# Performance work log

Measured on AMD Instinct MI355X. Metric: run time of the kernel, lower is better.

## Reference

```python
import jax, jax.numpy as jnp
import numpy as np

UNITS = 256


def setup_inputs() -> dict:
    key = jax.random.key(0)
    ks = jax.random.split(key, 9)
    B, H, W, C = 8, 64, 64, UNITS
    x = jax.random.normal(ks[0], (B, H, W, C), dtype=jnp.float32)
    # 1x1 Conv2D == per-pixel linear: weight [C_in, C_out], bias [C_out]
    def lin(k):
        return jax.random.normal(k, (C, UNITS), dtype=jnp.float32) * (2.0 / C) ** 0.5
    return {
        "x": x,
        "wq": lin(ks[1]), "bq": jnp.zeros((UNITS,), jnp.float32),
        "wk": lin(ks[2]), "bk": jnp.zeros((UNITS,), jnp.float32),
        "wv": lin(ks[3]), "bv": jnp.zeros((UNITS,), jnp.float32),
        "wp": lin(ks[4]), "bp": jnp.zeros((UNITS,), jnp.float32),
    }


def reference(x, wq, bq, wk, bk, wv, bv, wp, bp):
    B, H, W, C = x.shape
    N = H * W
    scale = jnp.asarray(UNITS, jnp.float32) ** -0.5
    xf = x.reshape(B, N, C)  # 1x1 conv == matmul over channels
    q = xf @ wq + bq
    k = xf @ wk + bk
    v = xf @ wv + bv
    # (b,h,w,c)x(b,H,W,c)->(b,h,w,H,W) flattened to (b,N,N)
    scores = jnp.einsum('bnc,bmc->bnm', q, k) * scale
    attn = jax.nn.softmax(scores, axis=-1)
    out = jnp.einsum('bnm,bmc->bnc', attn, v)
    proj = out @ wp + bp
    return x + proj.reshape(B, H, W, UNITS)
```

## Files before the change

kernel.cpp:

```cpp
#include <hip/hip_runtime.h>


typedef _Float16 half8 __attribute__((ext_vector_type(8)));
typedef _Float16 half4 __attribute__((ext_vector_type(4)));
typedef float f32x4 __attribute__((ext_vector_type(4)));
typedef float f32x16 __attribute__((ext_vector_type(16)));
typedef unsigned int u32x4 __attribute__((ext_vector_type(4)));
typedef unsigned int u32x2 __attribute__((ext_vector_type(2)));

#define MFMA16(a, b, c) __builtin_amdgcn_mfma_f32_16x16x32_f16((a), (b), (c), 0, 0, 0)
#define MFMA32(a, b, c) __builtin_amdgcn_mfma_f32_32x32x16_f16((a), (b), (c), 0, 0, 0)

#if __has_builtin(__builtin_amdgcn_exp2f)
#define EXP2(x) __builtin_amdgcn_exp2f(x)
#else
#define EXP2(x) exp2f(x)
#endif

#define QSCALE 0.09016843898f
#define ESHIFT 11.5415603f

__device__ __forceinline__ void lds_load16(const void* g, void* l) {
    __builtin_amdgcn_global_load_lds(
        (const __attribute__((address_space(1))) unsigned int*)g,
        (__attribute__((address_space(3))) unsigned int*)l, 16, 0, 0);
}

__global__ __launch_bounds__(256)
void wt_prep(const float* __restrict__ w0, const float* __restrict__ w1,
             const float* __restrict__ w2, const float* __restrict__ w3,
             _Float16* __restrict__ outw)
{
    __shared__ _Float16 sT[64 * 72];
    const int z = blockIdx.z;
    const float* W = (z == 0) ? w0 : (z == 1) ? w1 : (z == 2) ? w2 : w3;
    _Float16* O = outw + z * 65536;
    const int kb = blockIdx.x * 64, nb = blockIdx.y * 64;
    const int t = threadIdx.x;
    const int r = t >> 4, c4 = (t & 15) * 4;
#pragma unroll
    for (int i = 0; i < 4; ++i) {
        f32x4 ld = *(const f32x4*)(W + (size_t)(kb + r + i * 16) * 256 + nb + c4);
#pragma unroll
        for (int j = 0; j < 4; ++j) sT[(c4 + j) * 72 + r + i * 16] = (_Float16)ld[j];
    }
    __syncthreads();
#pragma unroll
    for (int i = 0; i < 4; ++i) {
        int n = r + i * 16;
        *(u32x2*)&O[(size_t)(nb + n) * 256 + kb + c4] = *(const u32x2*)&sT[n * 72 + c4];
    }
}

__global__ __launch_bounds__(256)
void qkv_gemm(const float* __restrict__ x, const _Float16* __restrict__ wt,
              const float* __restrict__ bq, const float* __restrict__ bk,
              const float* __restrict__ bv,
              _Float16* __restrict__ qo, _Float16* __restrict__ ko,
              _Float16* __restrict__ vo)
{
    __shared__ _Float16 smem[4 * 2560];
    _Float16* sA = smem;

    const int tid  = threadIdx.x;
    const int w    = tid >> 6;
    const int lane = tid & 63;
    const int quad = lane >> 4;
    const int l16  = lane & 15;
    const int m0   = blockIdx.x * 64;
    const int n0   = blockIdx.y * 64;
    const int rS = tid >> 2, cS = (tid & 3) << 3;

    const float* ap = x + (size_t)(m0 + rS) * 256 + cS;
    f32x4 a0 = *(const f32x4*)ap, a1 = *(const f32x4*)(ap + 4);
    u32x4 bst[3];
#pragma unroll
    for (int o = 0; o < 3; ++o)
        bst[o] = *(const u32x4*)(wt + o * 65536 + (size_t)(n0 + rS) * 256 + cS);

    f32x4 zero4 = {0.f, 0.f, 0.f, 0.f};
    f32x4 acc[3][4];
#pragma unroll
    for (int o = 0; o < 3; ++o)
#pragma unroll
        for (int mt = 0; mt < 4; ++mt) acc[o][mt] = zero4;

    for (int it = 0; it < 8; ++it) {
        __syncthreads();
        half8 t;
#pragma unroll
        for (int j = 0; j < 4; ++j) { t[j] = (_Float16)a0[j]; t[j + 4] = (_Float16)a1[j]; }
        *(half8*)&sA[rS * 40 + cS] = t;
#pragma unroll
        for (int o = 0; o < 3; ++o)
            *(u32x4*)&smem[2560 * (o + 1) + rS * 40 + cS] = bst[o];
        __syncthreads();
        if (it < 7) {
            int k0 = (it + 1) * 32;
            const float* ap2 = x + (size_t)(m0 + rS) * 256 + k0 + cS;
            a0 = *(const f32x4*)ap2; a1 = *(const f32x4*)(ap2 + 4);
#pragma unroll
            for (int o = 0; o < 3; ++o)
                bst[o] = *(const u32x4*)(wt + o * 65536 + (size_t)(n0 + rS) * 256 + k0 + cS);
        }
        half8 af[4];
#pragma unroll
        for (int mt = 0; mt < 4; ++mt)
            af[mt] = *(const half8*)&sA[(mt * 16 + l16) * 40 + quad * 8];
#pragma unroll
        for (int o = 0; o < 3; ++o) {
            half8 bf = *(const half8*)&smem[2560 * (o + 1) + (16 * w + l16) * 40 + quad * 8];
#pragma unroll
            for (int mt = 0; mt < 4; ++mt)
                acc[o][mt] = MFMA16(af[mt], bf, acc[o][mt]);
        }
    }

    const int col = n0 + 16 * w + l16;
#pragma unroll
    for (int mt = 0; mt < 4; ++mt) {
#pragma unroll
        for (int reg = 0; reg < 4; ++reg) {
            int row = m0 + 16 * mt + quad * 4 + reg;
            qo[(size_t)row * 256 + col] = (_Float16)((acc[0][mt][reg] + bq[col]) * QSCALE);
            ko[(size_t)row * 256 + col] = (_Float16)(acc[1][mt][reg] + bk[col]);
        }
    }
    __syncthreads();
    _Float16* sT = smem;
#pragma unroll
    for (int mt = 0; mt < 4; ++mt)
#pragma unroll
        for (int reg = 0; reg < 4; ++reg)
            sT[(16 * w + l16) * 72 + 16 * mt + quad * 4 + reg] =
                (_Float16)(acc[2][mt][reg] + bv[col]);
    __syncthreads();
    int ch = tid >> 2, po = (tid & 3) << 4;
    int bb = m0 >> 12, pix = m0 & 4095;
    _Float16* dst = vo + (size_t)bb * 1048576 + (size_t)(n0 + ch) * 4096 + pix + po;
    *(u32x4*)dst       = *(const u32x4*)&sT[ch * 72 + po];
    *(u32x4*)(dst + 8) = *(const u32x4*)&sT[ch * 72 + po + 8];
}

__global__ __launch_bounds__(256)
void proj_gemm(const _Float16* __restrict__ opart, const float* __restrict__ lpart,
               const _Float16* __restrict__ Wt, const float* __restrict__ bias,
               const float* __restrict__ resid, float* __restrict__ out)
{
    __shared__ _Float16 smem[2 * 2560];
    _Float16* sA = smem;
    _Float16* sB = smem + 2560;

    const int tid  = threadIdx.x;
    const int w    = tid >> 6;
    const int lane = tid & 63;
    const int quad = lane >> 4;
    const int l16  = lane & 15;
    const int m0   = blockIdx.x * 64;
    const int n0   = blockIdx.y * 64;
    const int rS = tid >> 2, cS = (tid & 3) << 3;

    const _Float16* o1p = opart;
    const _Float16* o2p = opart + 8388608;
    const int row = m0 + rS;
    const float inv = 1.0f / (lpart[row] + lpart[32768 + row]);

    u32x4 a1v = *(const u32x4*)(o1p + (size_t)row * 256 + cS);
    u32x4 a2v = *(const u32x4*)(o2p + (size_t)row * 256 + cS);
    u32x4 bst = *(const u32x4*)(Wt + (size_t)(n0 + rS) * 256 + cS);

    f32x4 zero4 = {0.f, 0.f, 0.f, 0.f};
    f32x4 acc[4] = {zero4, zero4, zero4, zero4};

    for (int it = 0; it < 8; ++it) {
        __syncthreads();
        {
            half8 h1 = *(half8*)&a1v, h2 = *(half8*)&a2v, t;
#pragma unroll
            for (int j = 0; j < 8; ++j)
                t[j] = (_Float16)(((float)h1[j] + (float)h2[j]) * inv);
            *(half8*)&sA[rS * 40 + cS] = t;
        }
        *(u32x4*)&sB[rS * 40 + cS] = bst;
        __syncthreads();
        if (it < 7) {
            int k0 = (it + 1) * 32;
            a1v = *(const u32x4*)(o1p + (size_t)row * 256 + k0 + cS);
            a2v = *(const u32x4*)(o2p + (size_t)row * 256 + k0 + cS);
            bst = *(const u32x4*)(Wt + (size_t)(n0 + rS) * 256 + k0 + cS);
        }
        half8 af = *(const half8*)&sA[(16 * w + l16) * 40 + quad * 8];
#pragma unroll
        for (int nt = 0; nt < 4; ++nt) {
            half8 bf = *(const half8*)&sB[(nt * 16 + l16) * 40 + quad * 8];
            acc[nt] = MFMA16(af, bf, acc[nt]);
        }
    }
#pragma unroll
    for (int nt = 0; nt < 4; ++nt) {
#pragma unroll
        for (int reg = 0; reg < 4; ++reg) {
            int orow = m0 + 16 * w + quad * 4 + reg;
            int col = n0 + nt * 16 + l16;
            out[(size_t)orow * 256 + col] =
                acc[nt][reg] + bias[col] + resid[(size_t)orow * 256 + col];
        }
    }
}

__global__ __launch_bounds__(512, 2)
void attn_kernel(const _Float16* __restrict__ q, const _Float16* __restrict__ k,
                 const _Float16* __restrict__ vt, _Float16* __restrict__ opart,
                 float* __restrict__ lpart)
{
    extern __shared__ char smem[];
    char* sKb = smem;
    char* sVb = smem + 32768;

    const int tid  = threadIdx.x;
    const int w    = tid >> 6;
    const int lane = tid & 63;
    const int l31  = lane & 31;
    const int hi   = lane >> 5;
    const int kh   = blockIdx.x & 1;
    const int qg   = (blockIdx.x >> 1) & 15;
    const int b    = blockIdx.x >> 5;

    char* sPw = smem + 65536 + w * 2560;

    const _Float16* kb = k  + (size_t)b * 1048576 + (size_t)kh * 524288;
    const _Float16* vb = vt + (size_t)b * 1048576 + kh * 2048;
    const int rowbase = qg * 256 + w * 32;

    half8 qf[16];
    {
        const _Float16* q0 = q + (size_t)(b * 4096 + rowbase + l31) * 256 + hi * 8;
#pragma unroll
        for (int s = 0; s < 16; ++s) qf[s] = *(const half8*)(q0 + s * 16);
    }

    f32x16 o[8];
#pragma unroll
    for (int i = 0; i < 8; ++i)
#pragma unroll
        for (int j = 0; j < 16; ++j) o[i][j] = 0.f;
    float ls = 0.f;

    const int koffL = l31 * 256 + hi * 8;

#pragma unroll
    for (int j = 0; j < 2; ++j) {
        int s = w * 2 + j;
        lds_load16(kb + koffL + s * 16, sKb + s * 1024);
        int ct = s >> 1, ks = s & 1;
        lds_load16(vb + (size_t)(32 * ct + l31) * 4096 + 16 * ks + 8 * hi,
                   sVb + s * 1024);
    }

    for (int kt = 0; kt < 64; ++kt) {
        const int p = kt & 1;
        __syncthreads();

        if (kt < 63) {
            const _Float16* ktb = kb + (size_t)(kt + 1) * 8192;
            const _Float16* vtb = vb + (kt + 1) * 32;
            char* dK = sKb + (1 - p) * 16384;
            char* dV = sVb + (1 - p) * 16384;
#pragma unroll
            for (int j = 0; j < 2; ++j) {
                int s = w * 2 + j;
                lds_load16(ktb + koffL + s * 16, dK + s * 1024);
                int ct = s >> 1, ks = s & 1;
                lds_load16(vtb + (size_t)(32 * ct + l31) * 4096 + 16 * ks + 8 * hi,
                           dV + s * 1024);
            }
        }

        const char* K = sKb + p * 16384;
        const char* V = sVb + p * 16384;

        f32x16 saA, saB;
#pragma unroll
        for (int j = 0; j < 16; ++j) { saA[j] = 0.f; saB[j] = 0.f; }
#pragma unroll
        for (int s = 0; s < 16; s += 2) {
            half8 a0 = *(const half8*)(K + s * 1024 + lane * 16);
            half8 a1 = *(const half8*)(K + (s + 1) * 1024 + lane * 16);
            saA = MFMA32(a0, qf[s], saA);
            saB = MFMA32(a1, qf[s + 1], saB);
        }

#pragma unroll
        for (int rb = 0; rb < 4; ++rb) {
            float p0 = EXP2(saA[rb * 4 + 0] + saB[rb * 4 + 0] - ESHIFT);
            float p1 = EXP2(saA[rb * 4 + 1] + saB[rb * 4 + 1] - ESHIFT);
            float p2 = EXP2(saA[rb * 4 + 2] + saB[rb * 4 + 2] - ESHIFT);
            float p3 = EXP2(saA[rb * 4 + 3] + saB[rb * 4 + 3] - ESHIFT);
            ls += (p0 + p1) + (p2 + p3);
            half4 t;
            t[0] = (_Float16)p0; t[1] = (_Float16)p1;
            t[2] = (_Float16)p2; t[3] = (_Float16)p3;
            *(half4*)(sPw + l31 * 80 + (8 * rb + 4 * hi) * 2) = t;
        }
        __asm__ volatile("s_waitcnt lgkmcnt(0)" ::: "memory");
        half8 pf0 = *(const half8*)(sPw + l31 * 80 + hi * 16);
        half8 pf1 = *(const half8*)(sPw + l31 * 80 + 32 + hi * 16);

#pragma unroll
        for (int ct = 0; ct < 8; ++ct) {
            half8 b0 = *(const half8*)(V + (ct * 2 + 0) * 1024 + lane * 16);
            half8 b1 = *(const half8*)(V + (ct * 2 + 1) * 1024 + lane * 16);
            o[ct] = MFMA32(pf0, b0, o[ct]);
            o[ct] = MFMA32(pf1, b1, o[ct]);
        }
    }

    ls += __shfl_xor(ls, 32);
    _Float16* po = opart + (size_t)kh * 8388608 + (size_t)(b * 4096 + rowbase) * 256;
    float* pl = lpart + kh * 32768 + b * 4096 + rowbase;
    if (hi == 0) pl[l31] = ls;
#pragma unroll
    for (int ct = 0; ct < 8; ++ct) {
#pragma unroll
        for (int reg = 0; reg < 16; ++reg) {
            int row = (reg & 3) + 8 * (reg >> 2) + 4 * hi;
            po[(size_t)row * 256 + ct * 32 + l31] = (_Float16)o[ct][reg];
        }
    }
}

extern "C" void kernel_launch(void* const* d_in, const int* in_sizes, int n_in,
                              void* d_out, int out_size, void* d_ws, size_t ws_size,
                              hipStream_t stream) {
    const float* x  = (const float*)d_in[0];
    const float* wq = (const float*)d_in[1];
    const float* bq = (const float*)d_in[2];
    const float* wk = (const float*)d_in[3];
    const float* bk = (const float*)d_in[4];
    const float* wv = (const float*)d_in[5];
    const float* bv = (const float*)d_in[6];
    const float* wp = (const float*)d_in[7];
    const float* bp = (const float*)d_in[8];

    _Float16* qws  = (_Float16*)d_ws;
    _Float16* kws  = qws + 8388608;
    _Float16* vtws = kws + 8388608;
    _Float16* ows  = vtws + 8388608;
    _Float16* wt   = ows + 16777216;
    float*    lws  = (float*)(wt + 262144);

    dim3 blk(256);

    (void)hipFuncSetAttribute((const void*)attn_kernel,
                              hipFuncAttributeMaxDynamicSharedMemorySize, 86016);

    wt_prep<<<dim3(4, 4, 4), blk, 0, stream>>>(wq, wk, wv, wp, wt);
    qkv_gemm<<<dim3(512, 4), blk, 0, stream>>>(x, wt, bq, bk, bv, qws, kws, vtws);
    attn_kernel<<<dim3(256), dim3(512), 86016, stream>>>(qws, kws, vtws, ows, lws);
    proj_gemm<<<dim3(512, 4), blk, 0, stream>>>(ows, lws, wt + 196608, bp, x, (float*)d_out);
}
```

Before: 290.7 us.

## Stage two KV tiles per barrier and pass P through permlane swaps

The attention loop now loads two 32-key K/V tiles per stage into doubled LDS buffers, which halves the number of block-wide barriers. The softmax probabilities are packed with cvt_pkrtz and rearranged into MFMA operand layout with permlane32_swap instead of a store to LDS, a wait and a reload. MFMA sections are also wrapped in s_setprio to favour matrix issue. Dynamic LDS grows to 128 KB, which limits occupancy to one block per CU, and the packed conversion rounds toward zero rather than to nearest.

```diff
diff --git a/kernel.cpp b/kernel.cpp
--- a/kernel.cpp
+++ b/kernel.cpp
@@ -215,7 +215,7 @@
 {
     extern __shared__ char smem[];
     char* sKb = smem;
-    char* sVb = smem + 32768;
+    char* sVb = smem + 65536;
 
     const int tid  = threadIdx.x;
     const int w    = tid >> 6;
@@ -226,8 +226,6 @@
     const int qg   = (blockIdx.x >> 1) & 15;
     const int b    = blockIdx.x >> 5;
 
-    char* sPw = smem + 65536 + w * 2560;
-
     const _Float16* kb = k  + (size_t)b * 1048576 + (size_t)kh * 524288;
     const _Float16* vb = vt + (size_t)b * 1048576 + kh * 2048;
     const int rowbase = qg * 256 + w * 32;
@@ -248,70 +246,80 @@
 
     const int koffL = l31 * 256 + hi * 8;
 
-#pragma unroll
-    for (int j = 0; j < 2; ++j) {
-        int s = w * 2 + j;
-        lds_load16(kb + koffL + s * 16, sKb + s * 1024);
-        int ct = s >> 1, ks = s & 1;
-        lds_load16(vb + (size_t)(32 * ct + l31) * 4096 + 16 * ks + 8 * hi,
-                   sVb + s * 1024);
-    }
-
-    for (int kt = 0; kt < 64; ++kt) {
-        const int p = kt & 1;
-        __syncthreads();
-
-        if (kt < 63) {
-            const _Float16* ktb = kb + (size_t)(kt + 1) * 8192;
-            const _Float16* vtb = vb + (kt + 1) * 32;
-            char* dK = sKb + (1 - p) * 16384;
-            char* dV = sVb + (1 - p) * 16384;
+    auto stage2 = [&](int T, char* dK, char* dV) {
+#pragma unroll
+        for (int tt = 0; tt < 2; ++tt) {
+            const _Float16* ktb = kb + (size_t)(2 * T + tt) * 8192;
+            const _Float16* vtb = vb + (2 * T + tt) * 32;
 #pragma unroll
             for (int j = 0; j < 2; ++j) {
                 int s = w * 2 + j;
-                lds_load16(ktb + koffL + s * 16, dK + s * 1024);
+                lds_load16(ktb + koffL + s * 16, dK + tt * 16384 + s * 1024);
                 int ct = s >> 1, ks = s & 1;
                 lds_load16(vtb + (size_t)(32 * ct + l31) * 4096 + 16 * ks + 8 * hi,
-                           dV + s * 1024);
+                           dV + tt * 16384 + s * 1024);
             }
         }
-
-        const char* K = sKb + p * 16384;
-        const char* V = sVb + p * 16384;
-
-        f32x16 saA, saB;
-#pragma unroll
-        for (int j = 0; j < 16; ++j) { saA[j] = 0.f; saB[j] = 0.f; }
-#pragma unroll
-        for (int s = 0; s < 16; s += 2) {
-            half8 a0 = *(const half8*)(K + s * 1024 + lane * 16);
-            half8 a1 = *(const half8*)(K + (s + 1) * 1024 + lane * 16);
-            saA = MFMA32(a0, qf[s], saA);
-            saB = MFMA32(a1, qf[s + 1], saB);
-        }
-
-#pragma unroll
-        for (int rb = 0; rb < 4; ++rb) {
-            float p0 = EXP2(saA[rb * 4 + 0] + saB[rb * 4 + 0] - ESHIFT);
-            float p1 = EXP2(saA[rb * 4 + 1] + saB[rb * 4 + 1] - ESHIFT);
-            float p2 = EXP2(saA[rb * 4 + 2] + saB[rb * 4 + 2] - ESHIFT);
-            float p3 = EXP2(saA[rb * 4 + 3] + saB[rb * 4 + 3] - ESHIFT);
-            ls += (p0 + p1) + (p2 + p3);
-            half4 t;
-            t[0] = (_Float16)p0; t[1] = (_Float16)p1;
-            t[2] = (_Float16)p2; t[3] = (_Float16)p3;
-            *(half4*)(sPw + l31 * 80 + (8 * rb + 4 * hi) * 2) = t;
-        }
-        __asm__ volatile("s_waitcnt lgkmcnt(0)" ::: "memory");
-        half8 pf0 = *(const half8*)(sPw + l31 * 80 + hi * 16);
-        half8 pf1 = *(const half8*)(sPw + l31 * 80 + 32 + hi * 16);
-
-#pragma unroll
-        for (int ct = 0; ct < 8; ++ct) {
-            half8 b0 = *(const half8*)(V + (ct * 2 + 0) * 1024 + lane * 16);
-            half8 b1 = *(const half8*)(V + (ct * 2 + 1) * 1024 + lane * 16);
-            o[ct] = MFMA32(pf0, b0, o[ct]);
-            o[ct] = MFMA32(pf1, b1, o[ct]);
+    };
+
+    stage2(0, sKb, sVb);
+
+    for (int T = 0; T < 32; ++T) {
+        const int p = T & 1;
+        __syncthreads();
+
+        if (T < 31)
+            stage2(T + 1, sKb + (1 - p) * 32768, sVb + (1 - p) * 32768);
+
+#pragma unroll
+        for (int tt = 0; tt < 2; ++tt) {
+            const char* K = sKb + p * 32768 + tt * 16384;
+            const char* V = sVb + p * 32768 + tt * 16384;
+
+            f32x16 saA, saB;
+#pragma unroll
+            for (int j = 0; j < 16; ++j) { saA[j] = 0.f; saB[j] = 0.f; }
+            __builtin_amdgcn_s_setprio(1);
+#pragma unroll
+            for (int s = 0; s < 16; s += 2) {
+                half8 a0 = *(const half8*)(K + s * 1024 + lane * 16);
+                half8 a1 = *(const half8*)(K + (s + 1) * 1024 + lane * 16);
+                saA = MFMA32(a0, qf[s], saA);
+                saB = MFMA32(a1, qf[s + 1], saB);
+            }
+            __builtin_amdgcn_s_setprio(0);
+
+            unsigned int c[8];
+#pragma unroll
+            for (int qq = 0; qq < 4; ++qq) {
+                float p0 = EXP2(saA[qq * 4 + 0] + saB[qq * 4 + 0] - ESHIFT);
+                float p1 = EXP2(saA[qq * 4 + 1] + saB[qq * 4 + 1] - ESHIFT);
+                float p2 = EXP2(saA[qq * 4 + 2] + saB[qq * 4 + 2] - ESHIFT);
+                float p3 = EXP2(saA[qq * 4 + 3] + saB[qq * 4 + 3] - ESHIFT);
+                ls += (p0 + p1) + (p2 + p3);
+                c[2 * qq]     = __builtin_bit_cast(unsigned int,
+                                    __builtin_amdgcn_cvt_pkrtz(p0, p1));
+                c[2 * qq + 1] = __builtin_bit_cast(unsigned int,
+                                    __builtin_amdgcn_cvt_pkrtz(p2, p3));
+            }
+            u32x2 s0 = __builtin_amdgcn_permlane32_swap(c[0], c[2], false, false);
+            u32x2 s1 = __builtin_amdgcn_permlane32_swap(c[1], c[3], false, false);
+            u32x2 s2 = __builtin_amdgcn_permlane32_swap(c[4], c[6], false, false);
+            u32x2 s3 = __builtin_amdgcn_permlane32_swap(c[5], c[7], false, false);
+            u32x4 w0 = {s0[0], s1[0], s0[1], s1[1]};
+            u32x4 w1 = {s2[0], s3[0], s2[1], s3[1]};
+            half8 pf0 = __builtin_bit_cast(half8, w0);
+            half8 pf1 = __builtin_bit_cast(half8, w1);
+
+            __builtin_amdgcn_s_setprio(1);
+#pragma unroll
+            for (int ct = 0; ct < 8; ++ct) {
+                half8 b0 = *(const half8*)(V + (ct * 2 + 0) * 1024 + lane * 16);
+                half8 b1 = *(const half8*)(V + (ct * 2 + 1) * 1024 + lane * 16);
+                o[ct] = MFMA32(pf0, b0, o[ct]);
+                o[ct] = MFMA32(pf1, b1, o[ct]);
+            }
+            __builtin_amdgcn_s_setprio(0);
         }
     }
 
@@ -352,10 +360,10 @@
     dim3 blk(256);
 
     (void)hipFuncSetAttribute((const void*)attn_kernel,
-                              hipFuncAttributeMaxDynamicSharedMemorySize, 86016);
+                              hipFuncAttributeMaxDynamicSharedMemorySize, 131072);
 
     wt_prep<<<dim3(4, 4, 4), blk, 0, stream>>>(wq, wk, wv, wp, wt);
     qkv_gemm<<<dim3(512, 4), blk, 0, stream>>>(x, wt, bq, bk, bv, qws, kws, vtws);
-    attn_kernel<<<dim3(256), dim3(512), 86016, stream>>>(qws, kws, vtws, ows, lws);
+    attn_kernel<<<dim3(256), dim3(512), 131072, stream>>>(qws, kws, vtws, ows, lws);
     proj_gemm<<<dim3(512, 4), blk, 0, stream>>>(ows, lws, wt + 196608, bp, x, (float*)d_out);
 }
```

Result: no change. 289.5 us (-0.4%).
